# Performance work log

Measured on AMD Instinct MI355X. Metric: run time of the kernel, lower is better.

Reference implementation:

```python
import jax, jax.numpy as jnp
import numpy as np

NEG_INF = float(np.finfo(np.float32).min)
CHUNK = 8
EPS = 1e-6
NOISE_STD = 1.0
SHARP = 1.0


def exclusive_cumsum(x):
    # [a,b,c] -> [0,a,a+b]
    return jnp.cumsum(jnp.pad(x[:, :-1], ((0, 0), (1, 0))), axis=1)


def moving_sum(x, back, forward):
    # x: [B, K]; out[i] = sum x[i-back : i+forward+1], via cumsum difference
    w = back + forward + 1
    xp = jnp.pad(x, ((0, 0), (back, forward)))
    cs = jnp.pad(jnp.cumsum(xp, axis=1), ((0, 0), (1, 0)))
    return cs[:, w:] - cs[:, :-w]


def setup_inputs() -> dict:
    key = jax.random.key(0)
    ks = jax.random.split(key, 12)
    B, K, D, A = 64, 2000, 512, 512
    s = 0.02
    inp = {
        'key': jax.random.normal(ks[0], (B, K, D), jnp.float32),
        'value': jax.random.normal(ks[1], (B, K, D), jnp.float32),
        'query': jax.random.normal(ks[2], (B, 1, D), jnp.float32),
        'mask': jnp.ones((B, 1, K), jnp.int32),
        'aw_prev': jnp.zeros((B, K), jnp.float32).at[:, 0].set(1.0),
        'noise': jax.random.normal(ks[3], (B, K), jnp.float32),
        'Wk_mono': jax.random.normal(ks[4], (D, A), jnp.float32) * s,
        'bk_mono': jnp.zeros((A,), jnp.float32),
        'Wq_mono': jax.random.normal(ks[5], (D, A), jnp.float32) * s,
        'bq_mono': jnp.zeros((A,), jnp.float32),
        'r': jnp.full((1,), -4.0, jnp.float32),
        'Wk_chunk': jax.random.normal(ks[6], (D, A), jnp.float32) * s,
        'bk_chunk': jnp.zeros((A,), jnp.float32),
        'Wq_chunk': jax.random.normal(ks[7], (D, A), jnp.float32) * s,
        'bq_chunk': jnp.zeros((A,), jnp.float32),
    }
    return inp


def reference(key, value, query, mask, aw_prev, noise,
              Wk_mono, bk_mono, Wq_mono, bq_mono, r,
              Wk_chunk, bk_chunk, Wq_chunk, bq_chunk):
    B, K, _ = key.shape
    adim = Wk_mono.shape[1]
    scale = jnp.sqrt(jnp.asarray(adim, jnp.float32))
    m = mask.reshape(B, K) != 0  # qlen == 1

    # ---- monotonic energy (scaled_dot) ----
    k_m = key @ Wk_mono + bk_mono              # [B,K,A]
    q_m = query @ Wq_mono + bq_mono            # [B,1,A]
    e_mono = jnp.einsum('bqa,bka->bk', q_m, k_m) / scale + r[0]
    e_mono = jnp.where(m, e_mono, NEG_INF)

    # ---- parallel-mode monotonic alignment ----
    p = jax.nn.sigmoid(e_mono + noise * NOISE_STD)             # p_choose_i
    cumprod_1mp = jnp.exp(exclusive_cumsum(jnp.log(jnp.clip(1.0 - p, EPS, 1.0))))
    alpha = p * cumprod_1mp * jnp.cumsum(
        aw_prev / jnp.clip(cumprod_1mp, EPS, 1.0), axis=1)     # [B,K]

    # ---- chunkwise attention ----
    k_c = key @ Wk_chunk + bk_chunk
    q_c = query @ Wq_chunk + bq_chunk
    e_c = jnp.einsum('bqa,bka->bk', q_c, k_c) / scale
    e_c = jnp.where(m, e_c, NEG_INF)
    e_c = e_c - jnp.max(e_c, axis=1, keepdims=True)
    sm_exp = jnp.clip(jnp.exp(e_c), 1e-5, None)
    denom = moving_sum(sm_exp, CHUNK - 1, 0)
    beta = sm_exp * moving_sum(alpha * SHARP / denom, 0, CHUNK - 1)  # [B,K]

    # ---- context vector ----
    cv = jnp.einsum('bk,bkd->bd', beta, value)[:, None, :]     # [B,1,D]
    return cv, alpha
```

## Files before the change

### kernel.cpp

```cpp
#include <hip/hip_runtime.h>
#include <hip/hip_bf16.h>

#define B_N    64
#define K_LEN  2000
#define D_DIM  512
#define NEG_INF (-3.402823466e38f)
#define EPS_C  1e-6f
#define INV_SCALE (1.0f/22.62741699796952f)

__global__ __launch_bounds__(256) void qproj_kernel(
    const float* __restrict__ query,
    const float* __restrict__ Wq_m, const float* __restrict__ bq_m,
    const float* __restrict__ Wq_c, const float* __restrict__ bq_c,
    float* __restrict__ q_all)
{
    const int b = blockIdx.x, br = blockIdx.y;
    const float* W = br ? Wq_c : Wq_m;
    const float* bias = br ? bq_c : bq_m;
    __shared__ float qs[D_DIM];
    for (int i = threadIdx.x; i < D_DIM; i += 256) qs[i] = query[(size_t)b*D_DIM + i];
    __syncthreads();
    for (int a = threadIdx.x; a < D_DIM; a += 256) {
        float acc = bias[a];
        for (int d = 0; d < D_DIM; ++d) acc = fmaf(qs[d], W[(size_t)d*D_DIM + a], acc);
        q_all[((size_t)b*2 + br)*D_DIM + a] = acc;
    }
}

__global__ __launch_bounds__(256) void vproj_kernel(
    const float* __restrict__ q_all,
    const float* __restrict__ Wk_m, const float* __restrict__ bk_m,
    const float* __restrict__ Wk_c, const float* __restrict__ bk_c,
    const float* __restrict__ r,
    float* __restrict__ v_all, float* __restrict__ c_all)
{
    const int b = blockIdx.x, br = blockIdx.y, t = threadIdx.x;
    const float* W = br ? Wk_c : Wk_m;
    const float* bias = br ? bk_c : bk_m;
    __shared__ float qs[D_DIM];
    __shared__ float red[256];
    for (int i = t; i < D_DIM; i += 256) qs[i] = q_all[((size_t)b*2 + br)*D_DIM + i];
    __syncthreads();
    for (int d = t; d < D_DIM; d += 256) {
        const float4* row = (const float4*)(W + (size_t)d*D_DIM);
        const float4* q4 = (const float4*)qs;
        float acc = 0.f;
        #pragma unroll 4
        for (int a4 = 0; a4 < D_DIM/4; ++a4) {
            float4 w = row[a4], q = q4[a4];
            acc = fmaf(w.x, q.x, acc); acc = fmaf(w.y, q.y, acc);
            acc = fmaf(w.z, q.z, acc); acc = fmaf(w.w, q.w, acc);
        }
        v_all[((size_t)b*2 + br)*D_DIM + d] = acc * INV_SCALE;
    }
    float part = 0.f;
    for (int a = t; a < D_DIM; a += 256) part = fmaf(qs[a], bias[a], part);
    red[t] = part; __syncthreads();
    for (int s = 128; s; s >>= 1) { if (t < s) red[t] += red[t + s]; __syncthreads(); }
    if (t == 0) c_all[b*2 + br] = red[0] * INV_SCALE + (br ? 0.f : r[0]);
}

__global__ __launch_bounds__(256) void energy_kernel(
    const float* __restrict__ key, const int* __restrict__ mask,
    const float* __restrict__ v_all, const float* __restrict__ c_all,
    float* __restrict__ e_mono, float* __restrict__ e_c)
{
    const int b = blockIdx.x;
    const int kb0 = blockIdx.y * 125;
    const int kend = kb0 + 125;
    const int lane = threadIdx.x & 63;
    const int wave = threadIdx.x >> 6;
    const float4* vm4 = (const float4*)(v_all + ((size_t)b*2 + 0)*D_DIM);
    const float4* vc4 = (const float4*)(v_all + ((size_t)b*2 + 1)*D_DIM);
    const float4 vmA = vm4[lane*2], vmB = vm4[lane*2 + 1];
    const float4 vcA = vc4[lane*2], vcB = vc4[lane*2 + 1];
    const float cm = c_all[b*2 + 0], cc = c_all[b*2 + 1];

    for (int k = kb0 + wave; k < kend; k += 4) {
        const float4* kr = (const float4*)(key + ((size_t)b*K_LEN + k)*D_DIM);
        float4 ka = kr[lane*2], kb4 = kr[lane*2 + 1];
        float dm = 0.f, dc = 0.f;
        dm = fmaf(ka.x, vmA.x, dm); dm = fmaf(ka.y, vmA.y, dm);
        dm = fmaf(ka.z, vmA.z, dm); dm = fmaf(ka.w, vmA.w, dm);
        dm = fmaf(kb4.x, vmB.x, dm); dm = fmaf(kb4.y, vmB.y, dm);
        dm = fmaf(kb4.z, vmB.z, dm); dm = fmaf(kb4.w, vmB.w, dm);
        dc = fmaf(ka.x, vcA.x, dc); dc = fmaf(ka.y, vcA.y, dc);
        dc = fmaf(ka.z, vcA.z, dc); dc = fmaf(ka.w, vcA.w, dc);
        dc = fmaf(kb4.x, vcB.x, dc); dc = fmaf(kb4.y, vcB.y, dc);
        dc = fmaf(kb4.z, vcB.z, dc); dc = fmaf(kb4.w, vcB.w, dc);
        #pragma unroll
        for (int off = 32; off; off >>= 1) {
            dm += __shfl_xor(dm, off);
            dc += __shfl_xor(dc, off);
        }
        if (lane == 0) {
            const size_t gk = (size_t)b*K_LEN + k;
            const bool mk = mask[gk] != 0;
            e_mono[gk] = mk ? dm + cm : NEG_INF;
            e_c[gk]    = mk ? dc + cc : NEG_INF;
        }
    }
}

__global__ __launch_bounds__(256) void scan_kernel(
    const float* __restrict__ e_mono_g, const float* __restrict__ e_c_g,
    const float* __restrict__ noise, const float* __restrict__ aw_prev,
    float* __restrict__ alpha_out, float* __restrict__ beta_out)
{
    const int b = blockIdx.x, t = threadIdx.x;
    __shared__ float sp[2048];
    __shared__ float scp[2048];
    __shared__ float sal[2048];
    __shared__ float sse[2048];
    __shared__ float su[2048];
    __shared__ float scan[256];

    const float* em = e_mono_g + (size_t)b*K_LEN;
    const float* ec = e_c_g   + (size_t)b*K_LEN;
    const float* nz = noise   + (size_t)b*K_LEN;
    const float* aw = aw_prev + (size_t)b*K_LEN;

    for (int k = t; k < 2048; k += 256) {
        float p = 0.f, lg = 0.f, ecv = NEG_INF;
        if (k < K_LEN) {
            float e = em[k] + nz[k];
            p = 1.f / (1.f + expf(-e));
            float om = fminf(fmaxf(1.f - p, EPS_C), 1.f);
            lg = logf(om);
            ecv = ec[k];
        }
        sp[k] = p; scp[k] = lg; sse[k] = ecv;
    }
    __syncthreads();

    const int base = t*8;
    float ex[8]; float run = 0.f;
    #pragma unroll
    for (int j = 0; j < 8; ++j) { ex[j] = run; run += scp[base + j]; }
    scan[t] = run; __syncthreads();
    for (int off = 1; off < 256; off <<= 1) {
        float x = (t >= off) ? scan[t - off] : 0.f; __syncthreads();
        scan[t] += x; __syncthreads();
    }
    const float pre = scan[t] - run;

    float t2i[8]; float run2 = 0.f;
    #pragma unroll
    for (int j = 0; j < 8; ++j) {
        int k = base + j;
        float cp = expf(pre + ex[j]);
        scp[k] = cp;
        float t2 = 0.f;
        if (k < K_LEN) t2 = aw[k] / fminf(fmaxf(cp, EPS_C), 1.f);
        run2 += t2; t2i[j] = run2;
    }
    __syncthreads();
    scan[t] = run2; __syncthreads();
    for (int off = 1; off < 256; off <<= 1) {
        float x = (t >= off) ? scan[t - off] : 0.f; __syncthreads();
        scan[t] += x; __syncthreads();
    }
    const float pre2 = scan[t] - run2;
    #pragma unroll
    for (int j = 0; j < 8; ++j) {
        int k = base + j;
        float al = sp[k] * scp[k] * (pre2 + t2i[j]);
        sal[k] = al;
        if (k < K_LEN) alpha_out[(size_t)b*K_LEN + k] = al;
    }

    float mx = NEG_INF;
    for (int k = t; k < 2048; k += 256) mx = fmaxf(mx, sse[k]);
    __syncthreads();
    scan[t] = mx; __syncthreads();
    for (int s = 128; s; s >>= 1) { if (t < s) scan[t] = fmaxf(scan[t], scan[t + s]); __syncthreads(); }
    mx = scan[0];

    for (int k = t; k < 2048; k += 256) {
        float se = 0.f;
        if (k < K_LEN) se = fmaxf(expf(sse[k] - mx), 1e-5f);
        sse[k] = se;
    }
    __syncthreads();
    for (int k = t; k < 2048; k += 256) {
        float u = 0.f;
        if (k < K_LEN) {
            float den = 0.f;
            int j0 = (k > 7) ? (k - 7) : 0;
            for (int j = j0; j <= k; ++j) den += sse[j];
            u = sal[k] / den;
        }
        su[k] = u;
    }
    __syncthreads();
    for (int k = t; k < K_LEN; k += 256) {
        float s2 = 0.f;
        #pragma unroll
        for (int j = 0; j < 8; ++j) s2 += su[k + j];
        beta_out[(size_t)b*K_LEN + k] = sse[k] * s2;
    }
}

__global__ __launch_bounds__(128) void cv_part_kernel(
    const float* __restrict__ value, const float* __restrict__ beta,
    float* __restrict__ partial)
{
    const int b = blockIdx.x, s = blockIdx.y, t = threadIdx.x;
    const int k0 = s * 50, k1 = k0 + 50;
    __shared__ float bs[50];
    if (t < 50) bs[t] = beta[(size_t)b*K_LEN + k0 + t];
    __syncthreads();
    float4 acc = {0.f, 0.f, 0.f, 0.f};
    for (int k = k0; k < k1; ++k) {
        float4 vv = ((const float4*)(value + ((size_t)b*K_LEN + k)*D_DIM))[t];
        float bb = bs[k - k0];
        acc.x = fmaf(bb, vv.x, acc.x); acc.y = fmaf(bb, vv.y, acc.y);
        acc.z = fmaf(bb, vv.z, acc.z); acc.w = fmaf(bb, vv.w, acc.w);
    }
    ((float4*)(partial + ((size_t)b*40 + s)*D_DIM))[t] = acc;
}

__global__ __launch_bounds__(256) void cv_reduce_kernel(
    const float* __restrict__ partial, float* __restrict__ cv)
{
    const int idx = blockIdx.x*256 + threadIdx.x;
    const int b = idx >> 9, d = idx & 511;
    float acc = 0.f;
    for (int s = 0; s < 40; ++s) acc += partial[((size_t)b*40 + s)*D_DIM + d];
    cv[idx] = acc;
}

extern "C" void kernel_launch(void* const* d_in, const int* in_sizes, int n_in,
                              void* d_out, int out_size, void* d_ws, size_t ws_size,
                              hipStream_t stream) {
    const float* key     = (const float*)d_in[0];
    const float* value   = (const float*)d_in[1];
    const float* query   = (const float*)d_in[2];
    const int*   mask    = (const int*)d_in[3];
    const float* aw_prev = (const float*)d_in[4];
    const float* noise   = (const float*)d_in[5];
    const float* Wk_m    = (const float*)d_in[6];
    const float* bk_m    = (const float*)d_in[7];
    const float* Wq_m    = (const float*)d_in[8];
    const float* bq_m    = (const float*)d_in[9];
    const float* r       = (const float*)d_in[10];
    const float* Wk_c    = (const float*)d_in[11];
    const float* bk_c    = (const float*)d_in[12];
    const float* Wq_c    = (const float*)d_in[13];
    const float* bq_c    = (const float*)d_in[14];

    float* out   = (float*)d_out;
    float* cv    = out;
    float* alpha = out + (size_t)B_N*D_DIM;

    float* ws      = (float*)d_ws;
    float* e_mono  = ws;
    float* e_c     = ws + 128000;
    float* beta    = ws + 256000;
    float* q_all   = ws + 384000;
    float* v_all   = ws + 449536;
    float* c_all   = ws + 515072;
    float* partial = ws + 515200;

    qproj_kernel<<<dim3(B_N, 2), 256, 0, stream>>>(query, Wq_m, bq_m, Wq_c, bq_c, q_all);
    vproj_kernel<<<dim3(B_N, 2), 256, 0, stream>>>(q_all, Wk_m, bk_m, Wk_c, bk_c, r, v_all, c_all);
    energy_kernel<<<dim3(B_N, 16), 256, 0, stream>>>(key, mask, v_all, c_all, e_mono, e_c);
    scan_kernel<<<B_N, 256, 0, stream>>>(e_mono, e_c, noise, aw_prev, alpha, beta);
    cv_part_kernel<<<dim3(B_N, 40), 128, 0, stream>>>(value, beta, partial);
    cv_reduce_kernel<<<32768/256, 256, 0, stream>>>(partial, cv);
}
```

Baseline: 624.9 us.

## Fuse query projections, unroll energy loop, use wave-shuffle scans, widen cv blocks

Merges the q-projection and v-projection kernels into one launch, and splits the q-projection dot product across four accumulators. The energy loop now handles two key rows per wave iteration to expose more memory parallelism. The scan kernel keeps per-thread values in registers and replaces its shared-memory Hillis-Steele scans and max reduction with wave shuffles plus a small cross-wave step. The context-vector partial kernel uses 256-thread blocks, each covering 100 keys in two halves combined through shared memory, which halves the number of partials to reduce. A leftover duplicate sigmoid line remains in the scan kernel, and it is harmless.

```diff
diff --git a/kernel.cpp b/kernel.cpp
--- a/kernel.cpp
+++ b/kernel.cpp
@@ -8,42 +8,40 @@
 #define EPS_C  1e-6f
 #define INV_SCALE (1.0f/22.62741699796952f)
 
-__global__ __launch_bounds__(256) void qproj_kernel(
+__global__ __launch_bounds__(256) void proj_kernel(
     const float* __restrict__ query,
     const float* __restrict__ Wq_m, const float* __restrict__ bq_m,
     const float* __restrict__ Wq_c, const float* __restrict__ bq_c,
-    float* __restrict__ q_all)
-{
-    const int b = blockIdx.x, br = blockIdx.y;
-    const float* W = br ? Wq_c : Wq_m;
-    const float* bias = br ? bq_c : bq_m;
-    __shared__ float qs[D_DIM];
-    for (int i = threadIdx.x; i < D_DIM; i += 256) qs[i] = query[(size_t)b*D_DIM + i];
-    __syncthreads();
-    for (int a = threadIdx.x; a < D_DIM; a += 256) {
-        float acc = bias[a];
-        for (int d = 0; d < D_DIM; ++d) acc = fmaf(qs[d], W[(size_t)d*D_DIM + a], acc);
-        q_all[((size_t)b*2 + br)*D_DIM + a] = acc;
-    }
-}
-
-__global__ __launch_bounds__(256) void vproj_kernel(
-    const float* __restrict__ q_all,
     const float* __restrict__ Wk_m, const float* __restrict__ bk_m,
     const float* __restrict__ Wk_c, const float* __restrict__ bk_c,
     const float* __restrict__ r,
     float* __restrict__ v_all, float* __restrict__ c_all)
 {
     const int b = blockIdx.x, br = blockIdx.y, t = threadIdx.x;
-    const float* W = br ? Wk_c : Wk_m;
-    const float* bias = br ? bk_c : bk_m;
+    const float* Wq = br ? Wq_c : Wq_m;
+    const float* bq = br ? bq_c : bq_m;
+    const float* Wk = br ? Wk_c : Wk_m;
+    const float* bk = br ? bk_c : bk_m;
     __shared__ float qs[D_DIM];
+    __shared__ float qv[D_DIM];
     __shared__ float red[256];
-    for (int i = t; i < D_DIM; i += 256) qs[i] = q_all[((size_t)b*2 + br)*D_DIM + i];
+    for (int i = t; i < D_DIM; i += 256) qs[i] = query[(size_t)b*D_DIM + i];
+    __syncthreads();
+    for (int a = t; a < D_DIM; a += 256) {
+        float a0 = 0.f, a1 = 0.f, a2 = 0.f, a3 = 0.f;
+        #pragma unroll 4
+        for (int d = 0; d < D_DIM; d += 4) {
+            a0 = fmaf(qs[d+0], Wq[(size_t)(d+0)*D_DIM + a], a0);
+            a1 = fmaf(qs[d+1], Wq[(size_t)(d+1)*D_DIM + a], a1);
+            a2 = fmaf(qs[d+2], Wq[(size_t)(d+2)*D_DIM + a], a2);
+            a3 = fmaf(qs[d+3], Wq[(size_t)(d+3)*D_DIM + a], a3);
+        }
+        qv[a] = (a0 + a1) + (a2 + a3) + bq[a];
+    }
     __syncthreads();
     for (int d = t; d < D_DIM; d += 256) {
-        const float4* row = (const float4*)(W + (size_t)d*D_DIM);
-        const float4* q4 = (const float4*)qs;
+        const float4* row = (const float4*)(Wk + (size_t)d*D_DIM);
+        const float4* q4 = (const float4*)qv;
         float acc = 0.f;
         #pragma unroll 4
         for (int a4 = 0; a4 < D_DIM/4; ++a4) {
@@ -54,7 +52,7 @@
         v_all[((size_t)b*2 + br)*D_DIM + d] = acc * INV_SCALE;
     }
     float part = 0.f;
-    for (int a = t; a < D_DIM; a += 256) part = fmaf(qs[a], bias[a], part);
+    for (int a = t; a < D_DIM; a += 256) part = fmaf(qv[a], bk[a], part);
     red[t] = part; __syncthreads();
     for (int s = 128; s; s >>= 1) { if (t < s) red[t] += red[t + s]; __syncthreads(); }
     if (t == 0) c_all[b*2 + br] = red[0] * INV_SCALE + (br ? 0.f : r[0]);
@@ -76,28 +74,46 @@
     const float4 vcA = vc4[lane*2], vcB = vc4[lane*2 + 1];
     const float cm = c_all[b*2 + 0], cc = c_all[b*2 + 1];
 
-    for (int k = kb0 + wave; k < kend; k += 4) {
-        const float4* kr = (const float4*)(key + ((size_t)b*K_LEN + k)*D_DIM);
-        float4 ka = kr[lane*2], kb4 = kr[lane*2 + 1];
-        float dm = 0.f, dc = 0.f;
-        dm = fmaf(ka.x, vmA.x, dm); dm = fmaf(ka.y, vmA.y, dm);
-        dm = fmaf(ka.z, vmA.z, dm); dm = fmaf(ka.w, vmA.w, dm);
-        dm = fmaf(kb4.x, vmB.x, dm); dm = fmaf(kb4.y, vmB.y, dm);
-        dm = fmaf(kb4.z, vmB.z, dm); dm = fmaf(kb4.w, vmB.w, dm);
-        dc = fmaf(ka.x, vcA.x, dc); dc = fmaf(ka.y, vcA.y, dc);
-        dc = fmaf(ka.z, vcA.z, dc); dc = fmaf(ka.w, vcA.w, dc);
-        dc = fmaf(kb4.x, vcB.x, dc); dc = fmaf(kb4.y, vcB.y, dc);
-        dc = fmaf(kb4.z, vcB.z, dc); dc = fmaf(kb4.w, vcB.w, dc);
+    for (int k = kb0 + wave; k < kend; k += 8) {
+        const int k2 = k + 4;
+        const bool has2 = (k2 < kend);
+        const float4* kr0 = (const float4*)(key + ((size_t)b*K_LEN + k)*D_DIM);
+        const float4* kr1 = (const float4*)(key + ((size_t)b*K_LEN + (has2 ? k2 : k))*D_DIM);
+        float4 a0 = kr0[lane*2], b0 = kr0[lane*2 + 1];
+        float4 a1 = kr1[lane*2], b1 = kr1[lane*2 + 1];
+        float dm0 = 0.f, dc0 = 0.f, dm1 = 0.f, dc1 = 0.f;
+        dm0 = fmaf(a0.x, vmA.x, dm0); dm0 = fmaf(a0.y, vmA.y, dm0);
+        dm0 = fmaf(a0.z, vmA.z, dm0); dm0 = fmaf(a0.w, vmA.w, dm0);
+        dm0 = fmaf(b0.x, vmB.x, dm0); dm0 = fmaf(b0.y, vmB.y, dm0);
+        dm0 = fmaf(b0.z, vmB.z, dm0); dm0 = fmaf(b0.w, vmB.w, dm0);
+        dc0 = fmaf(a0.x, vcA.x, dc0); dc0 = fmaf(a0.y, vcA.y, dc0);
+        dc0 = fmaf(a0.z, vcA.z, dc0); dc0 = fmaf(a0.w, vcA.w, dc0);
+        dc0 = fmaf(b0.x, vcB.x, dc0); dc0 = fmaf(b0.y, vcB.y, dc0);
+        dc0 = fmaf(b0.z, vcB.z, dc0); dc0 = fmaf(b0.w, vcB.w, dc0);
+        dm1 = fmaf(a1.x, vmA.x, dm1); dm1 = fmaf(a1.y, vmA.y, dm1);
+        dm1 = fmaf(a1.z, vmA.z, dm1); dm1 = fmaf(a1.w, vmA.w, dm1);
+        dm1 = fmaf(b1.x, vmB.x, dm1); dm1 = fmaf(b1.y, vmB.y, dm1);
+        dm1 = fmaf(b1.z, vmB.z, dm1); dm1 = fmaf(b1.w, vmB.w, dm1);
+        dc1 = fmaf(a1.x, vcA.x, dc1); dc1 = fmaf(a1.y, vcA.y, dc1);
+        dc1 = fmaf(a1.z, vcA.z, dc1); dc1 = fmaf(a1.w, vcA.w, dc1);
+        dc1 = fmaf(b1.x, vcB.x, dc1); dc1 = fmaf(b1.y, vcB.y, dc1);
+        dc1 = fmaf(b1.z, vcB.z, dc1); dc1 = fmaf(b1.w, vcB.w, dc1);
         #pragma unroll
         for (int off = 32; off; off >>= 1) {
-            dm += __shfl_xor(dm, off);
-            dc += __shfl_xor(dc, off);
+            dm0 += __shfl_xor(dm0, off); dc0 += __shfl_xor(dc0, off);
+            dm1 += __shfl_xor(dm1, off); dc1 += __shfl_xor(dc1, off);
         }
         if (lane == 0) {
-            const size_t gk = (size_t)b*K_LEN + k;
-            const bool mk = mask[gk] != 0;
-            e_mono[gk] = mk ? dm + cm : NEG_INF;
-            e_c[gk]    = mk ? dc + cc : NEG_INF;
+            size_t gk = (size_t)b*K_LEN + k;
+            bool mk = mask[gk] != 0;
+            e_mono[gk] = mk ? dm0 + cm : NEG_INF;
+            e_c[gk]    = mk ? dc0 + cc : NEG_INF;
+            if (has2) {
+                size_t gk2 = (size_t)b*K_LEN + k2;
+                bool mk2 = mask[gk2] != 0;
+                e_mono[gk2] = mk2 ? dm1 + cm : NEG_INF;
+                e_c[gk2]    = mk2 ? dc1 + cc : NEG_INF;
+            }
         }
     }
 }
@@ -108,73 +124,88 @@
     float* __restrict__ alpha_out, float* __restrict__ beta_out)
 {
     const int b = blockIdx.x, t = threadIdx.x;
-    __shared__ float sp[2048];
-    __shared__ float scp[2048];
+    const int lane = t & 63, wv = t >> 6;
     __shared__ float sal[2048];
     __shared__ float sse[2048];
     __shared__ float su[2048];
-    __shared__ float scan[256];
+    __shared__ float wsA[4], wsB[4], wsM[4];
 
     const float* em = e_mono_g + (size_t)b*K_LEN;
     const float* ec = e_c_g   + (size_t)b*K_LEN;
     const float* nz = noise   + (size_t)b*K_LEN;
     const float* aw = aw_prev + (size_t)b*K_LEN;
 
-    for (int k = t; k < 2048; k += 256) {
-        float p = 0.f, lg = 0.f, ecv = NEG_INF;
+    const int base = t*8;
+    float p[8], lg[8];
+    #pragma unroll
+    for (int j = 0; j < 8; ++j) {
+        const int k = base + j;
+        float pv = 0.f, lv = 0.f, ecv = NEG_INF;
         if (k < K_LEN) {
             float e = em[k] + nz[k];
-            p = 1.f / (1.f + expf(-e));
-            float om = fminf(fmaxf(1.f - p, EPS_C), 1.f);
-            lg = logf(om);
+            pv = 1.f / (1.f + __expf(-e) * 1.0f);
+            pv = 1.f / (1.f + expf(-e));
+            float om = fminf(fmaxf(1.f - pv, EPS_C), 1.f);
+            lv = logf(om);
             ecv = ec[k];
         }
-        sp[k] = p; scp[k] = lg; sse[k] = ecv;
-    }
-    __syncthreads();
-
-    const int base = t*8;
+        p[j] = pv; lg[j] = lv; sse[k] = ecv;
+    }
+
     float ex[8]; float run = 0.f;
     #pragma unroll
-    for (int j = 0; j < 8; ++j) { ex[j] = run; run += scp[base + j]; }
-    scan[t] = run; __syncthreads();
-    for (int off = 1; off < 256; off <<= 1) {
-        float x = (t >= off) ? scan[t - off] : 0.f; __syncthreads();
-        scan[t] += x; __syncthreads();
-    }
-    const float pre = scan[t] - run;
-
-    float t2i[8]; float run2 = 0.f;
+    for (int j = 0; j < 8; ++j) { ex[j] = run; run += lg[j]; }
+    float incl = run;
+    #pragma unroll
+    for (int off = 1; off < 64; off <<= 1) {
+        float v = __shfl_up(incl, off, 64);
+        if (lane >= off) incl += v;
+    }
+    if (lane == 63) wsA[wv] = incl;
+    __syncthreads();
+    float wpre = 0.f;
+    #pragma unroll
+    for (int w = 0; w < 4; ++w) if (w < wv) wpre += wsA[w];
+    const float pre = wpre + incl - run;
+
+    float cp[8], t2i[8]; float run2 = 0.f;
     #pragma unroll
     for (int j = 0; j < 8; ++j) {
-        int k = base + j;
-        float cp = expf(pre + ex[j]);
-        scp[k] = cp;
+        const int k = base + j;
+        float c = expf(pre + ex[j]);
+        cp[j] = c;
         float t2 = 0.f;
-        if (k < K_LEN) t2 = aw[k] / fminf(fmaxf(cp, EPS_C), 1.f);
+        if (k < K_LEN) t2 = aw[k] / fminf(fmaxf(c, EPS_C), 1.f);
         run2 += t2; t2i[j] = run2;
     }
-    __syncthreads();
-    scan[t] = run2; __syncthreads();
-    for (int off = 1; off < 256; off <<= 1) {
-        float x = (t >= off) ? scan[t - off] : 0.f; __syncthreads();
-        scan[t] += x; __syncthreads();
-    }
-    const float pre2 = scan[t] - run2;
+    float incl2 = run2;
+    #pragma unroll
+    for (int off = 1; off < 64; off <<= 1) {
+        float v = __shfl_up(incl2, off, 64);
+        if (lane >= off) incl2 += v;
+    }
+    if (lane == 63) wsB[wv] = incl2;
+    __syncthreads();
+    float wpre2 = 0.f;
+    #pragma unroll
+    for (int w = 0; w < 4; ++w) if (w < wv) wpre2 += wsB[w];
+    const float pre2 = wpre2 + incl2 - run2;
     #pragma unroll
     for (int j = 0; j < 8; ++j) {
-        int k = base + j;
-        float al = sp[k] * scp[k] * (pre2 + t2i[j]);
+        const int k = base + j;
+        float al = p[j] * cp[j] * (pre2 + t2i[j]);
         sal[k] = al;
         if (k < K_LEN) alpha_out[(size_t)b*K_LEN + k] = al;
     }
+    __syncthreads();
 
     float mx = NEG_INF;
     for (int k = t; k < 2048; k += 256) mx = fmaxf(mx, sse[k]);
-    __syncthreads();
-    scan[t] = mx; __syncthreads();
-    for (int s = 128; s; s >>= 1) { if (t < s) scan[t] = fmaxf(scan[t], scan[t + s]); __syncthreads(); }
-    mx = scan[0];
+    #pragma unroll
+    for (int off = 32; off; off >>= 1) mx = fmaxf(mx, __shfl_xor(mx, off));
+    if (lane == 0) wsM[wv] = mx;
+    __syncthreads();
+    mx = fmaxf(fmaxf(wsM[0], wsM[1]), fmaxf(wsM[2], wsM[3]));
 
     for (int k = t; k < 2048; k += 256) {
         float se = 0.f;
@@ -201,23 +232,31 @@
     }
 }
 
-__global__ __launch_bounds__(128) void cv_part_kernel(
+__global__ __launch_bounds__(256) void cv_part_kernel(
     const float* __restrict__ value, const float* __restrict__ beta,
     float* __restrict__ partial)
 {
     const int b = blockIdx.x, s = blockIdx.y, t = threadIdx.x;
-    const int k0 = s * 50, k1 = k0 + 50;
-    __shared__ float bs[50];
-    if (t < 50) bs[t] = beta[(size_t)b*K_LEN + k0 + t];
+    const int f4 = t & 127, half = t >> 7;
+    const int k0 = s * 100;
+    __shared__ float bs[100];
+    __shared__ float4 comb[128];
+    if (t < 100) bs[t] = beta[(size_t)b*K_LEN + k0 + t];
     __syncthreads();
     float4 acc = {0.f, 0.f, 0.f, 0.f};
-    for (int k = k0; k < k1; ++k) {
-        float4 vv = ((const float4*)(value + ((size_t)b*K_LEN + k)*D_DIM))[t];
+    for (int k = k0 + half; k < k0 + 100; k += 2) {
+        float4 vv = ((const float4*)(value + ((size_t)b*K_LEN + k)*D_DIM))[f4];
         float bb = bs[k - k0];
         acc.x = fmaf(bb, vv.x, acc.x); acc.y = fmaf(bb, vv.y, acc.y);
         acc.z = fmaf(bb, vv.z, acc.z); acc.w = fmaf(bb, vv.w, acc.w);
     }
-    ((float4*)(partial + ((size_t)b*40 + s)*D_DIM))[t] = acc;
+    if (half) comb[f4] = acc;
+    __syncthreads();
+    if (!half) {
+        float4 o = comb[f4];
+        acc.x += o.x; acc.y += o.y; acc.z += o.z; acc.w += o.w;
+        ((float4*)(partial + ((size_t)b*20 + s)*D_DIM))[f4] = acc;
+    }
 }
 
 __global__ __launch_bounds__(256) void cv_reduce_kernel(
@@ -226,7 +265,8 @@
     const int idx = blockIdx.x*256 + threadIdx.x;
     const int b = idx >> 9, d = idx & 511;
     float acc = 0.f;
-    for (int s = 0; s < 40; ++s) acc += partial[((size_t)b*40 + s)*D_DIM + d];
+    #pragma unroll
+    for (int s = 0; s < 20; ++s) acc += partial[((size_t)b*20 + s)*D_DIM + d];
     cv[idx] = acc;
 }
 
@@ -257,15 +297,15 @@
     float* e_mono  = ws;
     float* e_c     = ws + 128000;
     float* beta    = ws + 256000;
-    float* q_all   = ws + 384000;
-    float* v_all   = ws + 449536;
-    float* c_all   = ws + 515072;
-    float* partial = ws + 515200;
-
-    qproj_kernel<<<dim3(B_N, 2), 256, 0, stream>>>(query, Wq_m, bq_m, Wq_c, bq_c, q_all);
-    vproj_kernel<<<dim3(B_N, 2), 256, 0, stream>>>(q_all, Wk_m, bk_m, Wk_c, bk_c, r, v_all, c_all);
+    float* v_all   = ws + 384000;
+    float* c_all   = ws + 449536;
+    float* partial = ws + 449664;
+
+    proj_kernel<<<dim3(B_N, 2), 256, 0, stream>>>(query, Wq_m, bq_m, Wq_c, bq_c,
+                                                  Wk_m, bk_m, Wk_c, bk_c, r,
+                                                  v_all, c_all);
     energy_kernel<<<dim3(B_N, 16), 256, 0, stream>>>(key, mask, v_all, c_all, e_mono, e_c);
     scan_kernel<<<B_N, 256, 0, stream>>>(e_mono, e_c, noise, aw_prev, alpha, beta);
-    cv_part_kernel<<<dim3(B_N, 40), 128, 0, stream>>>(value, beta, partial);
+    cv_part_kernel<<<dim3(B_N, 20), 256, 0, stream>>>(value, beta, partial);
     cv_reduce_kernel<<<32768/256, 256, 0, stream>>>(partial, cv);
 }
```

New measurement: 613.2 us. About the same (-1.9%).
